# Optimization experiments

Measured on AMD Instinct MI355X. Metric: run time of the kernel, lower is better.

The kernel has to match this reference:

```python
import jax, jax.numpy as jnp
import numpy as np


def _schedule(epoch):
    # Mirrors SPLoss._adjust_N_ratio_q_t (epoch is a static Python int)
    if epoch <= 25:
        return 0.7, 2
    elif epoch <= 75:
        return 0.8, 0
    elif epoch <= 95:
        return 0.9, 0
    else:
        return 1.0, 0


def setup_inputs() -> dict:
    key = jax.random.key(0)
    k1, k2 = jax.random.split(key)
    B, C = 32768, 1000
    output = jax.random.normal(k1, (B, C), dtype=jnp.float32)
    target = jax.random.randint(k2, (B,), 0, C, dtype=jnp.int64)
    return {"output": output, "target": target, "epoch": 10}


def reference(output, target, epoch):
    N_ratio, q_t = _schedule(epoch)
    B = output.shape[0]
    # fused cross-entropy: log-softmax + per-sample gather
    logp = jax.nn.log_softmax(output, axis=-1)            # [B, C]
    ce_loss = -jnp.take_along_axis(logp, target[:, None], axis=1)[:, 0]  # [B]
    # sort-based quantile threshold
    sorted_ce = jnp.sort(ce_loss)                          # ascending
    lambda_t = sorted_ce[int(B * N_ratio)]
    # power reweight v_t = (1 - ce/lambda)^(1/(q_t-1)), zero past threshold, cap at 10
    exponent = 1.0 / (q_t - 1)
    v_t = (1.0 - ce_loss / lambda_t) ** exponent
    v_t = jnp.where(ce_loss >= lambda_t, 0.0, v_t)
    v_t = jnp.where(v_t >= 10.0, 10.0, v_t)
    return (ce_loss * v_t).mean()
```

## Files before the change

### kernel.cpp

```cpp
#include <hip/hip_runtime.h>
#include <math.h>


__device__ __forceinline__ unsigned f2u(float f) {
    unsigned u = __float_as_uint(f);
    return (u & 0x80000000u) ? ~u : (u | 0x80000000u);
}
__device__ __forceinline__ float u2f(unsigned u) {
    unsigned b = (u & 0x80000000u) ? (u & 0x7FFFFFFFu) : ~u;
    return __uint_as_float(b);
}

__global__ void ce_kernel(const float* __restrict__ x, const int* __restrict__ tgt,
                          const int* __restrict__ epoch_p, float* __restrict__ ce,
                          unsigned* __restrict__ hist, unsigned* __restrict__ state,
                          int B, int C)
{
    int tid = threadIdx.x;
    if (blockIdx.x == 0) {
        if (tid < 256) hist[tid] = 0u;
        if (tid == 0) {
            int e = epoch_p[0];
            double nr; int qt;
            if (e <= 25)      { nr = 0.7; qt = 2; }
            else if (e <= 75) { nr = 0.8; qt = 0; }
            else if (e <= 95) { nr = 0.9; qt = 0; }
            else              { nr = 1.0; qt = 0; }
            long long k = (long long)((double)B * nr);
            if (k > (long long)B - 1) k = B - 1;
            state[0] = 0u;
            state[1] = (unsigned)k;
            ((float*)state)[3] = 1.0f / (float)(qt - 1);
            ((float*)state)[4] = 0.0f;
        }
    }

    int lane = tid & 63;
    int row  = blockIdx.x * 4 + (tid >> 6);
    if (row >= B) return;

    const float* rp = x + (size_t)row * C;
    int C4 = C >> 2;
    float m = -INFINITY, s = 0.0f;

    const float4* p4 = (const float4*)rp;
    for (int i = lane; i < C4; i += 64) {
        float4 v = p4[i];
        float mx = fmaxf(fmaxf(v.x, v.y), fmaxf(v.z, v.w));
        if (mx > m) { s *= expf(m - mx); m = mx; }
        s += expf(v.x - m) + expf(v.y - m) + expf(v.z - m) + expf(v.w - m);
    }
    for (int i = (C4 << 2) + lane; i < C; i += 64) {
        float v = rp[i];
        if (v > m) { s *= expf(m - v); m = v; }
        s += expf(v - m);
    }

    for (int off = 32; off > 0; off >>= 1) {
        float mo = __shfl_down(m, off, 64);
        float so = __shfl_down(s, off, 64);
        float nm = fmaxf(m, mo);
        float a = (m  == nm) ? s  : s  * expf(m  - nm);
        float b = (mo == nm) ? so : so * expf(mo - nm);
        m = nm; s = a + b;
    }

    if (lane == 0) {
        int t = tgt[row];
        ce[row] = (m + logf(s)) - rp[t];
    }
}

__global__ void hist_kernel(const float* __restrict__ ce, unsigned* __restrict__ hist,
                            const unsigned* __restrict__ state, int B, int pass)
{
    __shared__ unsigned lh[256];
    int tid = threadIdx.x;
    lh[tid] = 0u;
    __syncthreads();

    int shift = 24 - 8 * pass;
    unsigned prefix = state[0];
    unsigned hm = (pass == 0) ? 0u : (0xFFFFFFFFu << (shift + 8));

    for (int i = blockIdx.x * blockDim.x + tid; i < B; i += gridDim.x * blockDim.x) {
        unsigned u = f2u(ce[i]);
        if ((u & hm) == (prefix & hm))
            atomicAdd(&lh[(u >> shift) & 0xFFu], 1u);
    }
    __syncthreads();
    if (lh[tid]) atomicAdd(&hist[tid], lh[tid]);
}

__global__ void scan_kernel(unsigned* __restrict__ hist, unsigned* __restrict__ state, int pass)
{
    __shared__ unsigned h[256];
    int tid = threadIdx.x;
    h[tid] = hist[tid];
    __syncthreads();
    hist[tid] = 0u;
    if (tid == 0) {
        unsigned k = state[1];
        unsigned cum = 0;
        int shift = 24 - 8 * pass;
        int bucket = 255;
        for (int i = 0; i < 256; ++i) {
            unsigned c = h[i];
            if (cum + c > k) { bucket = i; break; }
            cum += c;
        }
        state[1] = k - cum;
        unsigned prefix = state[0] | ((unsigned)bucket << shift);
        state[0] = prefix;
        if (pass == 3) ((float*)state)[2] = u2f(prefix);
    }
}

__global__ void reduce_kernel(const float* __restrict__ ce, unsigned* __restrict__ state, int B)
{
    float lam  = ((const float*)state)[2];
    float expo = ((const float*)state)[3];
    float* acc = &((float*)state)[4];

    float part = 0.0f;
    for (int i = blockIdx.x * blockDim.x + threadIdx.x; i < B; i += gridDim.x * blockDim.x) {
        float c = ce[i];
        float base = 1.0f - c / lam;
        float v = (expo == 1.0f) ? base : powf(base, expo);
        if (c >= lam)       v = 0.0f;
        else if (v >= 10.f) v = 10.0f;
        part += c * v;
    }
    for (int off = 32; off > 0; off >>= 1) part += __shfl_down(part, off, 64);

    __shared__ float wsum[4];
    int lane = threadIdx.x & 63, w = threadIdx.x >> 6;
    if (lane == 0) wsum[w] = part;
    __syncthreads();
    if (threadIdx.x == 0) {
        float t = 0.0f;
        int nw = (int)(blockDim.x >> 6);
        for (int i = 0; i < nw; ++i) t += wsum[i];
        atomicAdd(acc, t);
    }
}

__global__ void final_kernel(const unsigned* __restrict__ state, float* __restrict__ out, int B)
{
    out[0] = ((const float*)state)[4] / (float)B;
}

extern "C" void kernel_launch(void* const* d_in, const int* in_sizes, int n_in,
                              void* d_out, int out_size, void* d_ws, size_t ws_size,
                              hipStream_t stream)
{
    const float* x     = (const float*)d_in[0];
    const int*   tgt   = (const int*)d_in[1];
    const int*   epoch = (const int*)d_in[2];
    int B = in_sizes[1];
    int C = in_sizes[0] / B;

    float*    ce    = (float*)d_ws;
    unsigned* hist  = (unsigned*)((char*)d_ws + (size_t)B * 4);
    unsigned* state = hist + 256;

    int ceBlocks = (B + 3) / 4;
    ce_kernel<<<ceBlocks, 256, 0, stream>>>(x, tgt, epoch, ce, hist, state, B, C);

    for (int pass = 0; pass < 4; ++pass) {
        hist_kernel<<<128, 256, 0, stream>>>(ce, hist, state, B, pass);
        scan_kernel<<<1, 256, 0, stream>>>(hist, state, pass);
    }

    reduce_kernel<<<128, 256, 0, stream>>>(ce, state, B);
    final_kernel<<<1, 1, 0, stream>>>(state, (float*)d_out, B);
}
```

Before: 257.3 us.

## Fuse CE, radix select, and reduction into one kernel with last-block finish

Replaces the eleven-kernel pipeline (CE, four histogram/scan pass pairs, reduce, final) with one kernel. Each block computes CE for 16 rows, and the last block to arrive, found through an atomic counter, keeps all CE values in registers. That block runs the four radix-select passes with a shared-memory histogram and a wave-level scan, then does the weighted reduction itself. It also switches to fast __expf/__logf and replaces powf with a direct reciprocal or identity. The aim is to remove launch overhead and the global histogram round-trips. In exchange, the tail work is serialised onto a single block, the code hardcodes B ≤ 32768, and the fast math intrinsics are less precise.

```diff
diff --git a/kernel.cpp b/kernel.cpp
--- a/kernel.cpp
+++ b/kernel.cpp
@@ -1,6 +1,9 @@
 #include <hip/hip_runtime.h>
 #include <math.h>
 
+
+#define BLOCK 1024
+#define WPB   16
 
 __device__ __forceinline__ unsigned f2u(float f) {
     unsigned u = __float_as_uint(f);
@@ -11,143 +14,143 @@
     return __uint_as_float(b);
 }
 
-__global__ void ce_kernel(const float* __restrict__ x, const int* __restrict__ tgt,
-                          const int* __restrict__ epoch_p, float* __restrict__ ce,
-                          unsigned* __restrict__ hist, unsigned* __restrict__ state,
-                          int B, int C)
+__global__ __launch_bounds__(BLOCK) void sploss_kernel(
+        const float* __restrict__ x, const int* __restrict__ tgt,
+        const int* __restrict__ epoch_p,
+        unsigned* __restrict__ ceu, unsigned* __restrict__ counter,
+        float* __restrict__ out, int B, int C)
 {
-    int tid = threadIdx.x;
-    if (blockIdx.x == 0) {
-        if (tid < 256) hist[tid] = 0u;
-        if (tid == 0) {
-            int e = epoch_p[0];
-            double nr; int qt;
-            if (e <= 25)      { nr = 0.7; qt = 2; }
-            else if (e <= 75) { nr = 0.8; qt = 0; }
-            else if (e <= 95) { nr = 0.9; qt = 0; }
-            else              { nr = 1.0; qt = 0; }
-            long long k = (long long)((double)B * nr);
-            if (k > (long long)B - 1) k = B - 1;
-            state[0] = 0u;
-            state[1] = (unsigned)k;
-            ((float*)state)[3] = 1.0f / (float)(qt - 1);
-            ((float*)state)[4] = 0.0f;
+    const int tid  = threadIdx.x;
+    const int lane = tid & 63;
+    const int wave = tid >> 6;
+
+    int row = blockIdx.x * WPB + wave;
+    if (row < B) {
+        const float* rp = x + (size_t)row * C;
+        int t = tgt[row];
+        float tv = rp[t];
+        float m = -INFINITY, s = 0.0f;
+        const float4* p4 = (const float4*)rp;
+        int C4 = C >> 2;
+        for (int i = lane; i < C4; i += 64) {
+            float4 v = p4[i];
+            float mx = fmaxf(fmaxf(v.x, v.y), fmaxf(v.z, v.w));
+            if (mx > m) { s *= __expf(m - mx); m = mx; }
+            s += __expf(v.x - m) + __expf(v.y - m) + __expf(v.z - m) + __expf(v.w - m);
+        }
+        for (int i = (C4 << 2) + lane; i < C; i += 64) {
+            float v = rp[i];
+            if (v > m) { s *= __expf(m - v); m = v; }
+            s += __expf(v - m);
+        }
+        for (int off = 32; off > 0; off >>= 1) {
+            float mo = __shfl_down(m, off, 64);
+            float so = __shfl_down(s, off, 64);
+            float nm = fmaxf(m, mo);
+            float a = (m  == nm) ? s  : s  * __expf(m  - nm);
+            float b = (mo == nm) ? so : so * __expf(mo - nm);
+            m = nm; s = a + b;
+        }
+        if (lane == 0) {
+            float cev = (m + __logf(s)) - tv;
+            __hip_atomic_store(&ceu[row], f2u(cev),
+                               __ATOMIC_RELAXED, __HIP_MEMORY_SCOPE_AGENT);
         }
     }
 
-    int lane = tid & 63;
-    int row  = blockIdx.x * 4 + (tid >> 6);
-    if (row >= B) return;
+    __shared__ unsigned s_old;
+    __syncthreads();
+    if (tid == 0)
+        s_old = __hip_atomic_fetch_add(counter, 1u,
+                                       __ATOMIC_ACQ_REL, __HIP_MEMORY_SCOPE_AGENT);
+    __syncthreads();
+    if (s_old != gridDim.x - 1) return;
 
-    const float* rp = x + (size_t)row * C;
-    int C4 = C >> 2;
-    float m = -INFINITY, s = 0.0f;
+    int e = epoch_p[0];
+    double nr; int qt;
+    if (e <= 25)      { nr = 0.7; qt = 2; }
+    else if (e <= 75) { nr = 0.8; qt = 0; }
+    else if (e <= 95) { nr = 0.9; qt = 0; }
+    else              { nr = 1.0; qt = 0; }
+    long long kk = (long long)((double)B * nr);
+    if (kk > (long long)B - 1) kk = (long long)B - 1;
+    const bool inv = (qt != 2);
 
-    const float4* p4 = (const float4*)rp;
-    for (int i = lane; i < C4; i += 64) {
-        float4 v = p4[i];
-        float mx = fmaxf(fmaxf(v.x, v.y), fmaxf(v.z, v.w));
-        if (mx > m) { s *= expf(m - mx); m = mx; }
-        s += expf(v.x - m) + expf(v.y - m) + expf(v.z - m) + expf(v.w - m);
-    }
-    for (int i = (C4 << 2) + lane; i < C; i += 64) {
-        float v = rp[i];
-        if (v > m) { s *= expf(m - v); m = v; }
-        s += expf(v - m);
+    unsigned uv[32];
+#pragma unroll
+    for (int j = 0; j < 32; ++j) {
+        int i = tid + j * BLOCK;
+        uv[j] = (i < B) ? __hip_atomic_load(&ceu[i], __ATOMIC_RELAXED,
+                                            __HIP_MEMORY_SCOPE_AGENT)
+                        : 0xFFFFFFFFu;
     }
 
-    for (int off = 32; off > 0; off >>= 1) {
-        float mo = __shfl_down(m, off, 64);
-        float so = __shfl_down(s, off, 64);
-        float nm = fmaxf(m, mo);
-        float a = (m  == nm) ? s  : s  * expf(m  - nm);
-        float b = (mo == nm) ? so : so * expf(mo - nm);
-        m = nm; s = a + b;
+    __shared__ unsigned lh[256];
+    __shared__ unsigned s_prefix, s_k;
+    if (tid == 0) { s_prefix = 0u; s_k = (unsigned)kk; }
+
+    for (int p = 0; p < 4; ++p) {
+        if (tid < 256) lh[tid] = 0u;
+        __syncthreads();
+        const int shift = 24 - 8 * p;
+        const unsigned hm   = (p == 0) ? 0u : (0xFFFFFFFFu << (shift + 8));
+        const unsigned pref = s_prefix;
+#pragma unroll
+        for (int j = 0; j < 32; ++j) {
+            unsigned u = uv[j];
+            if ((u & hm) == (pref & hm))
+                atomicAdd(&lh[(u >> shift) & 255u], 1u);
+        }
+        __syncthreads();
+        if (wave == 0) {
+            unsigned c0 = lh[4 * lane], c1 = lh[4 * lane + 1];
+            unsigned c2 = lh[4 * lane + 2], c3 = lh[4 * lane + 3];
+            unsigned c4 = c0 + c1 + c2 + c3;
+            unsigned incl = c4;
+            for (int off = 1; off < 64; off <<= 1) {
+                unsigned tt = __shfl_up(incl, off, 64);
+                if (lane >= off) incl += tt;
+            }
+            unsigned excl = incl - c4;
+            unsigned kr = s_k;
+            unsigned long long bm = __ballot(excl <= kr && kr < excl + c4);
+            int L = __ffsll(bm) - 1;
+            if (lane == L) {
+                unsigned rem = kr - excl;
+                int b; unsigned cum;
+                if      (rem < c0)           { b = 0; cum = 0; }
+                else if (rem < c0 + c1)      { b = 1; cum = c0; }
+                else if (rem < c0 + c1 + c2) { b = 2; cum = c0 + c1; }
+                else                         { b = 3; cum = c0 + c1 + c2; }
+                s_k = rem - cum;
+                s_prefix = pref | ((unsigned)(4 * lane + b) << shift);
+            }
+        }
+        __syncthreads();
     }
 
-    if (lane == 0) {
-        int t = tgt[row];
-        ce[row] = (m + logf(s)) - rp[t];
-    }
-}
-
-__global__ void hist_kernel(const float* __restrict__ ce, unsigned* __restrict__ hist,
-                            const unsigned* __restrict__ state, int B, int pass)
-{
-    __shared__ unsigned lh[256];
-    int tid = threadIdx.x;
-    lh[tid] = 0u;
-    __syncthreads();
-
-    int shift = 24 - 8 * pass;
-    unsigned prefix = state[0];
-    unsigned hm = (pass == 0) ? 0u : (0xFFFFFFFFu << (shift + 8));
-
-    for (int i = blockIdx.x * blockDim.x + tid; i < B; i += gridDim.x * blockDim.x) {
-        unsigned u = f2u(ce[i]);
-        if ((u & hm) == (prefix & hm))
-            atomicAdd(&lh[(u >> shift) & 0xFFu], 1u);
-    }
-    __syncthreads();
-    if (lh[tid]) atomicAdd(&hist[tid], lh[tid]);
-}
-
-__global__ void scan_kernel(unsigned* __restrict__ hist, unsigned* __restrict__ state, int pass)
-{
-    __shared__ unsigned h[256];
-    int tid = threadIdx.x;
-    h[tid] = hist[tid];
-    __syncthreads();
-    hist[tid] = 0u;
-    if (tid == 0) {
-        unsigned k = state[1];
-        unsigned cum = 0;
-        int shift = 24 - 8 * pass;
-        int bucket = 255;
-        for (int i = 0; i < 256; ++i) {
-            unsigned c = h[i];
-            if (cum + c > k) { bucket = i; break; }
-            cum += c;
-        }
-        state[1] = k - cum;
-        unsigned prefix = state[0] | ((unsigned)bucket << shift);
-        state[0] = prefix;
-        if (pass == 3) ((float*)state)[2] = u2f(prefix);
-    }
-}
-
-__global__ void reduce_kernel(const float* __restrict__ ce, unsigned* __restrict__ state, int B)
-{
-    float lam  = ((const float*)state)[2];
-    float expo = ((const float*)state)[3];
-    float* acc = &((float*)state)[4];
-
+    const float lam = u2f(s_prefix);
     float part = 0.0f;
-    for (int i = blockIdx.x * blockDim.x + threadIdx.x; i < B; i += gridDim.x * blockDim.x) {
-        float c = ce[i];
+#pragma unroll
+    for (int j = 0; j < 32; ++j) {
+        int i = tid + j * BLOCK;
+        if (i >= B) continue;
+        float c = u2f(uv[j]);
         float base = 1.0f - c / lam;
-        float v = (expo == 1.0f) ? base : powf(base, expo);
+        float v = inv ? (1.0f / base) : base;
         if (c >= lam)       v = 0.0f;
         else if (v >= 10.f) v = 10.0f;
         part += c * v;
     }
     for (int off = 32; off > 0; off >>= 1) part += __shfl_down(part, off, 64);
-
-    __shared__ float wsum[4];
-    int lane = threadIdx.x & 63, w = threadIdx.x >> 6;
-    if (lane == 0) wsum[w] = part;
+    __shared__ float wsum[WPB];
+    if (lane == 0) wsum[wave] = part;
     __syncthreads();
-    if (threadIdx.x == 0) {
-        float t = 0.0f;
-        int nw = (int)(blockDim.x >> 6);
-        for (int i = 0; i < nw; ++i) t += wsum[i];
-        atomicAdd(acc, t);
+    if (tid == 0) {
+        float tot = 0.0f;
+        for (int i = 0; i < WPB; ++i) tot += wsum[i];
+        out[0] = tot / (float)B;
     }
-}
-
-__global__ void final_kernel(const unsigned* __restrict__ state, float* __restrict__ out, int B)
-{
-    out[0] = ((const float*)state)[4] / (float)B;
 }
 
 extern "C" void kernel_launch(void* const* d_in, const int* in_sizes, int n_in,
@@ -160,18 +163,12 @@
     int B = in_sizes[1];
     int C = in_sizes[0] / B;
 
-    float*    ce    = (float*)d_ws;
-    unsigned* hist  = (unsigned*)((char*)d_ws + (size_t)B * 4);
-    unsigned* state = hist + 256;
+    unsigned* ceu     = (unsigned*)d_ws;
+    unsigned* counter = ceu + B;
 
-    int ceBlocks = (B + 3) / 4;
-    ce_kernel<<<ceBlocks, 256, 0, stream>>>(x, tgt, epoch, ce, hist, state, B, C);
+    hipMemsetAsync(counter, 0, sizeof(unsigned), stream);
 
-    for (int pass = 0; pass < 4; ++pass) {
-        hist_kernel<<<128, 256, 0, stream>>>(ce, hist, state, B, pass);
-        scan_kernel<<<1, 256, 0, stream>>>(hist, state, pass);
-    }
-
-    reduce_kernel<<<128, 256, 0, stream>>>(ce, state, B);
-    final_kernel<<<1, 1, 0, stream>>>(state, (float*)d_out, B);
+    int blocks = (B + WPB - 1) / WPB;
+    sploss_kernel<<<blocks, BLOCK, 0, stream>>>(x, tgt, epoch, ceu, counter,
+                                                (float*)d_out, B, C);
 }
```

New measurement: 255.3 us. Within noise of the previous version (-0.8%).
